# Kernel optimization log

Measured on AMD Instinct MI355X. Metric: run time of the kernel, lower is better.

## Reference

```python
import jax, jax.numpy as jnp
import numpy as np

DIM = 1024

def setup_inputs() -> dict:
    key = jax.random.key(0)
    k1, k2, k3, k4, k5 = jax.random.split(key, 5)
    x = jax.random.normal(k1, (4, 2048, DIM), dtype=jnp.float32)
    w_qkv = jax.random.normal(k2, (DIM, 3 * DIM), dtype=jnp.float32) * (DIM ** -0.5)
    b_qkv = jax.random.normal(k3, (3 * DIM,), dtype=jnp.float32) * 0.02
    w_proj = jax.random.normal(k4, (DIM, DIM), dtype=jnp.float32) * (DIM ** -0.5)
    b_proj = jax.random.normal(k5, (DIM,), dtype=jnp.float32) * 0.02
    return {"x": x, "w_qkv": w_qkv, "b_qkv": b_qkv, "w_proj": w_proj, "b_proj": b_proj}

def reference(x, w_qkv, b_qkv, w_proj, b_proj):
    # qkv projection: [B, S, 3*D] -> chunk into q, k, v
    qkv = jnp.einsum('bsd,de->bse', x, w_qkv) + b_qkv
    q, k, v = jnp.split(qkv, 3, axis=-1)
    scale = jnp.asarray(DIM ** 0.5, dtype=x.dtype)  # note: module divides by dim**0.5
    attn = jnp.einsum('bqd,bkd->bqk', q, k) / scale  # [B, S, S]
    attn = jax.nn.softmax(attn, axis=-1)
    out = jnp.einsum('bqk,bkd->bqd', attn, v)
    return jnp.einsum('bsd,de->bse', out, w_proj) + b_proj
```

## Files before the change

kernel.cpp:

```cpp
#include <hip/hip_runtime.h>

typedef unsigned short u16;
typedef __attribute__((ext_vector_type(8))) unsigned short u16x8;
typedef __attribute__((ext_vector_type(8))) short s16x8;
typedef __attribute__((ext_vector_type(4))) float f32x4;

__device__ __forceinline__ u16 f2bf(float f) {
    union { float f; unsigned int u; } c; c.f = f;
    unsigned int u = c.u;
    u += 0x7fffu + ((u >> 16) & 1u);
    return (u16)(u >> 16);
}
__device__ __forceinline__ float bf2f(u16 h) {
    union { unsigned int u; float f; } c; c.u = ((unsigned int)h) << 16; return c.f;
}

__device__ __forceinline__ void gload16(const u16* g, u16* l) {
    __builtin_amdgcn_global_load_lds(
        (const __attribute__((address_space(1))) void*)g,
        (__attribute__((address_space(3))) void*)l, 16, 0, 0);
}

__global__ __launch_bounds__(256) void cast_f32_bf16(const float* __restrict__ in,
                                                     u16* __restrict__ out, int n8) {
    int i = blockIdx.x * 256 + threadIdx.x;
    if (i >= n8) return;
    const float4* p = (const float4*)in;
    float4 a = p[2 * i], b = p[2 * i + 1];
    u16x8 o;
    o[0] = f2bf(a.x); o[1] = f2bf(a.y); o[2] = f2bf(a.z); o[3] = f2bf(a.w);
    o[4] = f2bf(b.x); o[5] = f2bf(b.y); o[6] = f2bf(b.z); o[7] = f2bf(b.w);
    ((u16x8*)out)[i] = o;
}

__global__ __launch_bounds__(256) void transpose_cast_f32(const float* __restrict__ src,
                                                          u16* __restrict__ dst, int R, int C) {
    __shared__ u16 t[32][33];
    int tx = threadIdx.x & 31, ty = threadIdx.x >> 5;
    int c0 = blockIdx.x * 32, r0 = blockIdx.y * 32;
#pragma unroll
    for (int i = 0; i < 4; ++i)
        t[ty + i * 8][tx] = f2bf(src[(size_t)(r0 + ty + i * 8) * C + c0 + tx]);
    __syncthreads();
#pragma unroll
    for (int i = 0; i < 4; ++i)
        dst[(size_t)(c0 + ty + i * 8) * R + r0 + tx] = t[tx][ty + i * 8];
}

__global__ __launch_bounds__(256) void transpose_b16(const u16* __restrict__ src,
                                                     u16* __restrict__ dst, int R, int C) {
    src += (size_t)blockIdx.z * R * C;
    dst += (size_t)blockIdx.z * R * C;
    __shared__ u16 t[32][33];
    int tx = threadIdx.x & 31, ty = threadIdx.x >> 5;
    int c0 = blockIdx.x * 32, r0 = blockIdx.y * 32;
#pragma unroll
    for (int i = 0; i < 4; ++i)
        t[ty + i * 8][tx] = src[(size_t)(r0 + ty + i * 8) * C + c0 + tx];
    __syncthreads();
#pragma unroll
    for (int i = 0; i < 4; ++i)
        dst[(size_t)(c0 + ty + i * 8) * R + r0 + tx] = t[tx][ty + i * 8];
}

__global__ __launch_bounds__(256) void softmax_rows_b16(u16* __restrict__ S) {
    const int t = threadIdx.x;
    u16* row = S + (size_t)blockIdx.x * 2048;
    u16x8 a = ((const u16x8*)row)[t];
    float f[8];
#pragma unroll
    for (int j = 0; j < 8; ++j) f[j] = bf2f(a[j]);
    float m = fmaxf(fmaxf(fmaxf(f[0], f[1]), fmaxf(f[2], f[3])),
                    fmaxf(fmaxf(f[4], f[5]), fmaxf(f[6], f[7])));
#pragma unroll
    for (int o = 32; o >= 1; o >>= 1) m = fmaxf(m, __shfl_xor(m, o));
    __shared__ float sm[4], ss[4];
    if ((t & 63) == 0) sm[t >> 6] = m;
    __syncthreads();
    m = fmaxf(fmaxf(sm[0], sm[1]), fmaxf(sm[2], sm[3]));
    float s = 0.f;
#pragma unroll
    for (int j = 0; j < 8; ++j) { f[j] = __expf(f[j] - m); s += f[j]; }
#pragma unroll
    for (int o = 32; o >= 1; o >>= 1) s += __shfl_xor(s, o);
    if ((t & 63) == 0) ss[t >> 6] = s;
    __syncthreads();
    s = (ss[0] + ss[1]) + (ss[2] + ss[3]);
    float inv = 1.f / s;
    u16x8 o8;
#pragma unroll
    for (int j = 0; j < 8; ++j) o8[j] = f2bf(f[j] * inv);
    ((u16x8*)row)[t] = o8;
}

template<int EPI>
__global__ __launch_bounds__(256) void gemm128(
    const u16* __restrict__ A, const u16* __restrict__ Bt,
    int K, int ldA, int ldBt,
    const float* __restrict__ bias,
    float* __restrict__ outF, int ldOutF,
    u16* __restrict__ outH, int ldOutH,
    u16* __restrict__ Qo, u16* __restrict__ Ko, u16* __restrict__ Vo,
    size_t zA, size_t zBt, size_t zOut) {
    __shared__ u16 lds[2][16384];
    const int tid  = threadIdx.x;
    const int lane = tid & 63;
    const int wave = tid >> 6;
    const int wrow = wave >> 1, wcol = wave & 1;
    const int lrow = lane & 15;
    const int lkg  = lane >> 4;
    const int bm0  = blockIdx.x * 128;
    const int bn0  = blockIdx.y * 128;
    A  += zA  * blockIdx.z;
    Bt += zBt * blockIdx.z;

    const int srow = tid >> 3;
    const int ssc  = (((tid & 7) * 16) ^ ((srow & 7) << 4)) >> 1;
    const u16* aS[4];
    const u16* bS[4];
#pragma unroll
    for (int g = 0; g < 4; ++g) {
        aS[g] = A  + (size_t)(bm0 + g * 32 + srow) * ldA  + ssc;
        bS[g] = Bt + (size_t)(bn0 + g * 32 + srow) * ldBt + ssc;
    }
    const int dst = wave * 512;

#define STAGE(t, b)                                                   \
    _Pragma("unroll")                                                 \
    for (int g = 0; g < 4; ++g) {                                     \
        gload16(aS[g] + (size_t)(t) * 64, lds[b] + g * 2048 + dst);   \
        gload16(bS[g] + (size_t)(t) * 64, lds[b] + 8192 + g * 2048 + dst); \
    }

    const int sc0 = (lkg * 16) ^ ((lrow & 7) << 4);
    const int sc1 = (64 + lkg * 16) ^ ((lrow & 7) << 4);

    f32x4 acc[4][4] = {};
    const int NT = K >> 6;

    STAGE(0, 0);
    asm volatile("s_waitcnt vmcnt(0)" ::: "memory");
    __builtin_amdgcn_s_barrier();
    __builtin_amdgcn_sched_barrier(0);

    for (int t = 0; t < NT; ++t) {
        const int c = t & 1, o = c ^ 1;
        if (t + 1 < NT) STAGE(t + 1, o);
        const char* base = (const char*)lds[c];
        s16x8 ra[4][2], rb[4][2];
#pragma unroll
        for (int i = 0; i < 4; ++i) {
            const char* p = base + (wrow * 64 + i * 16 + lrow) * 128;
            ra[i][0] = *(const s16x8*)(p + sc0);
            ra[i][1] = *(const s16x8*)(p + sc1);
        }
#pragma unroll
        for (int j = 0; j < 4; ++j) {
            const char* p = base + 16384 + (wcol * 64 + j * 16 + lrow) * 128;
            rb[j][0] = *(const s16x8*)(p + sc0);
            rb[j][1] = *(const s16x8*)(p + sc1);
        }
#pragma unroll
        for (int ks = 0; ks < 2; ++ks)
#pragma unroll
            for (int i = 0; i < 4; ++i)
#pragma unroll
                for (int j = 0; j < 4; ++j)
                    acc[i][j] = __builtin_amdgcn_mfma_f32_16x16x32_bf16(
                        ra[i][ks], rb[j][ks], acc[i][j], 0, 0, 0);
        asm volatile("s_waitcnt vmcnt(0)" ::: "memory");
        __builtin_amdgcn_s_barrier();
        __builtin_amdgcn_sched_barrier(0);
    }
#undef STAGE

    if (zOut) outH += zOut * blockIdx.z;
#pragma unroll
    for (int i = 0; i < 4; ++i) {
        int row0 = bm0 + wrow * 64 + i * 16 + lkg * 4;
#pragma unroll
        for (int j = 0; j < 4; ++j) {
            int col = bn0 + wcol * 64 + j * 16 + lrow;
#pragma unroll
            for (int r = 0; r < 4; ++r) {
                int row = row0 + r;
                float v = acc[i][j][r];
                if constexpr (EPI == 0) {
                    v += bias[col];
                    if (col < 1024)       Qo[(size_t)row * 1024 + col] = f2bf(v * 0.03125f);
                    else if (col < 2048)  Ko[(size_t)row * 1024 + (col - 1024)] = f2bf(v);
                    else                  Vo[(size_t)row * 1024 + (col - 2048)] = f2bf(v);
                } else if constexpr (EPI == 2) {
                    outH[(size_t)row * ldOutH + col] = f2bf(v);
                } else {
                    outF[(size_t)row * ldOutF + col] = v + bias[col];
                }
            }
        }
    }
}

extern "C" void kernel_launch(void* const* d_in, const int* in_sizes, int n_in,
                              void* d_out, int out_size, void* d_ws, size_t ws_size,
                              hipStream_t stream) {
    const float* x      = (const float*)d_in[0];
    const float* w_qkv  = (const float*)d_in[1];
    const float* b_qkv  = (const float*)d_in[2];
    const float* w_proj = (const float*)d_in[3];
    const float* b_proj = (const float*)d_in[4];
    float* out = (float*)d_out;
    char* ws = (char*)d_ws;
    (void)in_sizes; (void)n_in; (void)out_size;

    const size_t MB16  = 16777216;
    const size_t BATCH = 2097152;
    const size_t SZB   = 4194304;

    if (ws_size >= 85983232) {
        u16* xb     = (u16*)(ws);
        u16* Qb     = (u16*)(ws + MB16);
        u16* Kb     = (u16*)(ws + 2 * MB16);
        u16* Vb     = (u16*)(ws + 3 * MB16);
        u16* wqkvT  = (u16*)(ws + 4 * MB16);
        u16* Vt     = xb;
        u16* Ob     = Qb;
        u16* Sb     = Vb;
        u16* wprojT = Kb;

        cast_f32_bf16<<<4096, 256, 0, stream>>>(x, xb, 1048576);
        transpose_cast_f32<<<dim3(96, 32), 256, 0, stream>>>(w_qkv, wqkvT, 1024, 3072);
        gemm128<0><<<dim3(64, 24), 256, 0, stream>>>(xb, wqkvT, 1024, 1024, 1024,
                                                     b_qkv, nullptr, 0, nullptr, 0,
                                                     Qb, Kb, Vb, 0, 0, 0);
        transpose_b16<<<dim3(32, 64, 4), 256, 0, stream>>>(Vb, Vt, 2048, 1024);
        gemm128<2><<<dim3(16, 16, 4), 256, 0, stream>>>(Qb, Kb, 1024, 1024, 1024,
                                                        nullptr, nullptr, 0, Sb, 2048,
                                                        nullptr, nullptr, nullptr,
                                                        BATCH, BATCH, SZB);
        softmax_rows_b16<<<8192, 256, 0, stream>>>(Sb);
        gemm128<2><<<dim3(16, 8, 4), 256, 0, stream>>>(Sb, Vt, 2048, 2048, 2048,
                                                       nullptr, nullptr, 0, Ob, 1024,
                                                       nullptr, nullptr, nullptr,
                                                       SZB, BATCH, BATCH);
        transpose_cast_f32<<<dim3(32, 32), 256, 0, stream>>>(w_proj, wprojT, 1024, 1024);
        gemm128<3><<<dim3(64, 8), 256, 0, stream>>>(Ob, wprojT, 1024, 1024, 1024,
                                                    b_proj, out, 1024, nullptr, 0,
                                                    nullptr, nullptr, nullptr, 0, 0, 0);
    } else {
        u16* xbB    = (u16*)(ws);
        u16* QbB    = (u16*)(ws + 4194304);
        u16* KbB    = (u16*)(ws + 8388608);
        u16* VbB    = (u16*)(ws + 12582912);
        u16* VtB    = (u16*)(ws + 16777216);
        u16* Sb     = (u16*)(ws + 20971520);
        u16* wqkvT  = (u16*)(ws + 37748736);
        u16* wprojT = (u16*)(ws + 44040192);
        u16* ObB    = xbB;

        transpose_cast_f32<<<dim3(96, 32), 256, 0, stream>>>(w_qkv, wqkvT, 1024, 3072);
        transpose_cast_f32<<<dim3(32, 32), 256, 0, stream>>>(w_proj, wprojT, 1024, 1024);
        for (int b = 0; b < 4; ++b) {
            cast_f32_bf16<<<1024, 256, 0, stream>>>(x + (size_t)b * BATCH, xbB, 262144);
            gemm128<0><<<dim3(16, 24), 256, 0, stream>>>(xbB, wqkvT, 1024, 1024, 1024,
                                                         b_qkv, nullptr, 0, nullptr, 0,
                                                         QbB, KbB, VbB, 0, 0, 0);
            transpose_b16<<<dim3(32, 64, 1), 256, 0, stream>>>(VbB, VtB, 2048, 1024);
            gemm128<2><<<dim3(16, 16), 256, 0, stream>>>(QbB, KbB, 1024, 1024, 1024,
                                                         nullptr, nullptr, 0, Sb, 2048,
                                                         nullptr, nullptr, nullptr, 0, 0, 0);
            softmax_rows_b16<<<2048, 256, 0, stream>>>(Sb);
            gemm128<2><<<dim3(16, 8), 256, 0, stream>>>(Sb, VtB, 2048, 2048, 2048,
                                                        nullptr, nullptr, 0, ObB, 1024,
                                                        nullptr, nullptr, nullptr, 0, 0, 0);
            gemm128<3><<<dim3(16, 8), 256, 0, stream>>>(ObB, wprojT, 1024, 1024, 1024,
                                                        b_proj, out + (size_t)b * BATCH, 1024,
                                                        nullptr, 0, nullptr, nullptr, nullptr,
                                                        0, 0, 0);
        }
    }
}
```

Measured before the change: 203.1 us.

## Fold output projection into V before attention and swizzle QKV GEMM blocks

Uses associativity, softmax(S)·(V·Wp) + b = softmax(S)·V·Wp + b, because softmax rows sum to one. The kernel precomputes (V·Wp + b_proj)^T per batch with a GEMM whose output is already transposed. This removes the separate V transpose kernel and the final projection GEMM, and the PV GEMM now writes fp32 output directly. It also adds a grouped block-index swizzle to the QKV GEMM for better cache locality. The precomputed Vp is stored in bf16, which adds one extra rounding step.

```diff
diff --git a/kernel.cpp b/kernel.cpp
--- a/kernel.cpp
+++ b/kernel.cpp
@@ -47,22 +47,6 @@
         dst[(size_t)(c0 + ty + i * 8) * R + r0 + tx] = t[tx][ty + i * 8];
 }
 
-__global__ __launch_bounds__(256) void transpose_b16(const u16* __restrict__ src,
-                                                     u16* __restrict__ dst, int R, int C) {
-    src += (size_t)blockIdx.z * R * C;
-    dst += (size_t)blockIdx.z * R * C;
-    __shared__ u16 t[32][33];
-    int tx = threadIdx.x & 31, ty = threadIdx.x >> 5;
-    int c0 = blockIdx.x * 32, r0 = blockIdx.y * 32;
-#pragma unroll
-    for (int i = 0; i < 4; ++i)
-        t[ty + i * 8][tx] = src[(size_t)(r0 + ty + i * 8) * C + c0 + tx];
-    __syncthreads();
-#pragma unroll
-    for (int i = 0; i < 4; ++i)
-        dst[(size_t)(c0 + ty + i * 8) * R + r0 + tx] = t[tx][ty + i * 8];
-}
-
 __global__ __launch_bounds__(256) void softmax_rows_b16(u16* __restrict__ S) {
     const int t = threadIdx.x;
     u16* row = S + (size_t)blockIdx.x * 2048;
@@ -93,7 +77,7 @@
     ((u16x8*)row)[t] = o8;
 }
 
-template<int EPI>
+template<int EPI, int SWZ>
 __global__ __launch_bounds__(256) void gemm128(
     const u16* __restrict__ A, const u16* __restrict__ Bt,
     int K, int ldA, int ldBt,
@@ -109,8 +93,17 @@
     const int wrow = wave >> 1, wcol = wave & 1;
     const int lrow = lane & 15;
     const int lkg  = lane >> 4;
-    const int bm0  = blockIdx.x * 128;
-    const int bn0  = blockIdx.y * 128;
+
+    int bx = blockIdx.x, by = blockIdx.y;
+    if constexpr (SWZ) {
+        int id = bx + gridDim.x * by;
+        int chunk = (gridDim.x * gridDim.y) >> 3;
+        int t2 = (id & 7) * chunk + (id >> 3);
+        bx = t2 / gridDim.y;
+        by = t2 % gridDim.y;
+    }
+    const int bm0 = bx * 128;
+    const int bn0 = by * 128;
     A  += zA  * blockIdx.z;
     Bt += zBt * blockIdx.z;
 
@@ -174,7 +167,8 @@
     }
 #undef STAGE
 
-    if (zOut) outH += zOut * blockIdx.z;
+    if constexpr (EPI == 1) outF += zOut * blockIdx.z;
+    else if constexpr (EPI == 2 || EPI == 4) outH += zOut * blockIdx.z;
 #pragma unroll
     for (int i = 0; i < 4; ++i) {
         int row0 = bm0 + wrow * 64 + i * 16 + lkg * 4;
@@ -190,10 +184,12 @@
                     if (col < 1024)       Qo[(size_t)row * 1024 + col] = f2bf(v * 0.03125f);
                     else if (col < 2048)  Ko[(size_t)row * 1024 + (col - 1024)] = f2bf(v);
                     else                  Vo[(size_t)row * 1024 + (col - 2048)] = f2bf(v);
+                } else if constexpr (EPI == 1) {
+                    outF[(size_t)row * ldOutF + col] = v;
                 } else if constexpr (EPI == 2) {
                     outH[(size_t)row * ldOutH + col] = f2bf(v);
                 } else {
-                    outF[(size_t)row * ldOutF + col] = v + bias[col];
+                    outH[(size_t)row * ldOutH + col] = f2bf(v + bias[row]);
                 }
             }
         }
@@ -215,6 +211,7 @@
     const size_t MB16  = 16777216;
     const size_t BATCH = 2097152;
     const size_t SZB   = 4194304;
+    const size_t VPB   = 2097152;
 
     if (ws_size >= 85983232) {
         u16* xb     = (u16*)(ws);
@@ -222,60 +219,57 @@
         u16* Kb     = (u16*)(ws + 2 * MB16);
         u16* Vb     = (u16*)(ws + 3 * MB16);
         u16* wqkvT  = (u16*)(ws + 4 * MB16);
-        u16* Vt     = xb;
-        u16* Ob     = Qb;
+        u16* wprojT = (u16*)(ws + 4 * MB16 + 6291456);
+        u16* Vpt    = xb;
         u16* Sb     = Vb;
-        u16* wprojT = Kb;
 
         cast_f32_bf16<<<4096, 256, 0, stream>>>(x, xb, 1048576);
         transpose_cast_f32<<<dim3(96, 32), 256, 0, stream>>>(w_qkv, wqkvT, 1024, 3072);
-        gemm128<0><<<dim3(64, 24), 256, 0, stream>>>(xb, wqkvT, 1024, 1024, 1024,
-                                                     b_qkv, nullptr, 0, nullptr, 0,
-                                                     Qb, Kb, Vb, 0, 0, 0);
-        transpose_b16<<<dim3(32, 64, 4), 256, 0, stream>>>(Vb, Vt, 2048, 1024);
-        gemm128<2><<<dim3(16, 16, 4), 256, 0, stream>>>(Qb, Kb, 1024, 1024, 1024,
-                                                        nullptr, nullptr, 0, Sb, 2048,
-                                                        nullptr, nullptr, nullptr,
-                                                        BATCH, BATCH, SZB);
+        transpose_cast_f32<<<dim3(32, 32), 256, 0, stream>>>(w_proj, wprojT, 1024, 1024);
+        gemm128<0, 1><<<dim3(64, 24), 256, 0, stream>>>(xb, wqkvT, 1024, 1024, 1024,
+                                                        b_qkv, nullptr, 0, nullptr, 0,
+                                                        Qb, Kb, Vb, 0, 0, 0);
+        gemm128<4, 0><<<dim3(8, 16, 4), 256, 0, stream>>>(wprojT, Vb, 1024, 1024, 1024,
+                                                          b_proj, nullptr, 0, Vpt, 2048,
+                                                          nullptr, nullptr, nullptr,
+                                                          0, BATCH, VPB);
+        gemm128<2, 0><<<dim3(16, 16, 4), 256, 0, stream>>>(Qb, Kb, 1024, 1024, 1024,
+                                                           nullptr, nullptr, 0, Sb, 2048,
+                                                           nullptr, nullptr, nullptr,
+                                                           BATCH, BATCH, SZB);
         softmax_rows_b16<<<8192, 256, 0, stream>>>(Sb);
-        gemm128<2><<<dim3(16, 8, 4), 256, 0, stream>>>(Sb, Vt, 2048, 2048, 2048,
-                                                       nullptr, nullptr, 0, Ob, 1024,
-                                                       nullptr, nullptr, nullptr,
-                                                       SZB, BATCH, BATCH);
-        transpose_cast_f32<<<dim3(32, 32), 256, 0, stream>>>(w_proj, wprojT, 1024, 1024);
-        gemm128<3><<<dim3(64, 8), 256, 0, stream>>>(Ob, wprojT, 1024, 1024, 1024,
-                                                    b_proj, out, 1024, nullptr, 0,
-                                                    nullptr, nullptr, nullptr, 0, 0, 0);
+        gemm128<1, 0><<<dim3(16, 8, 4), 256, 0, stream>>>(Sb, Vpt, 2048, 2048, 2048,
+                                                          nullptr, out, 1024, nullptr, 0,
+                                                          nullptr, nullptr, nullptr,
+                                                          SZB, VPB, BATCH);
     } else {
         u16* xbB    = (u16*)(ws);
         u16* QbB    = (u16*)(ws + 4194304);
         u16* KbB    = (u16*)(ws + 8388608);
         u16* VbB    = (u16*)(ws + 12582912);
-        u16* VtB    = (u16*)(ws + 16777216);
+        u16* VptB   = (u16*)(ws + 16777216);
         u16* Sb     = (u16*)(ws + 20971520);
-        u16* wqkvT  = (u16*)(ws + 37748736);
-        u16* wprojT = (u16*)(ws + 44040192);
-        u16* ObB    = xbB;
+        u16* wqkvT  = (u16*)(ws + 29360128);
+        u16* wprojT = (u16*)(ws + 35651584);
 
         transpose_cast_f32<<<dim3(96, 32), 256, 0, stream>>>(w_qkv, wqkvT, 1024, 3072);
         transpose_cast_f32<<<dim3(32, 32), 256, 0, stream>>>(w_proj, wprojT, 1024, 1024);
         for (int b = 0; b < 4; ++b) {
             cast_f32_bf16<<<1024, 256, 0, stream>>>(x + (size_t)b * BATCH, xbB, 262144);
-            gemm128<0><<<dim3(16, 24), 256, 0, stream>>>(xbB, wqkvT, 1024, 1024, 1024,
-                                                         b_qkv, nullptr, 0, nullptr, 0,
-                                                         QbB, KbB, VbB, 0, 0, 0);
-            transpose_b16<<<dim3(32, 64, 1), 256, 0, stream>>>(VbB, VtB, 2048, 1024);
-            gemm128<2><<<dim3(16, 16), 256, 0, stream>>>(QbB, KbB, 1024, 1024, 1024,
-                                                         nullptr, nullptr, 0, Sb, 2048,
-                                                         nullptr, nullptr, nullptr, 0, 0, 0);
+            gemm128<0, 0><<<dim3(16, 24), 256, 0, stream>>>(xbB, wqkvT, 1024, 1024, 1024,
+                                                            b_qkv, nullptr, 0, nullptr, 0,
+                                                            QbB, KbB, VbB, 0, 0, 0);
+            gemm128<4, 0><<<dim3(8, 16), 256, 0, stream>>>(wprojT, VbB, 1024, 1024, 1024,
+                                                           b_proj, nullptr, 0, VptB, 2048,
+                                                           nullptr, nullptr, nullptr, 0, 0, 0);
+            gemm128<2, 0><<<dim3(16, 16), 256, 0, stream>>>(QbB, KbB, 1024, 1024, 1024,
+                                                            nullptr, nullptr, 0, Sb, 2048,
+                                                            nullptr, nullptr, nullptr, 0, 0, 0);
             softmax_rows_b16<<<2048, 256, 0, stream>>>(Sb);
-            gemm128<2><<<dim3(16, 8), 256, 0, stream>>>(Sb, VtB, 2048, 2048, 2048,
-                                                        nullptr, nullptr, 0, ObB, 1024,
-                                                        nullptr, nullptr, nullptr, 0, 0, 0);
-            gemm128<3><<<dim3(16, 8), 256, 0, stream>>>(ObB, wprojT, 1024, 1024, 1024,
-                                                        b_proj, out + (size_t)b * BATCH, 1024,
-                                                        nullptr, 0, nullptr, nullptr, nullptr,
-                                                        0, 0, 0);
-        }
-    }
-}
+            gemm128<1, 0><<<dim3(16, 8), 256, 0, stream>>>(Sb, VptB, 2048, 2048, 2048,
+                                                           nullptr, out + (size_t)b * BATCH, 1024,
+                                                           nullptr, 0,
+                                                           nullptr, nullptr, nullptr, 0, 0, 0);
+        }
+    }
+}
```

New measurement: 203.4 us. Within noise of the previous version (+0.2%).
